# Optimization experiments

Measured on AMD Instinct MI355X. Metric: run time of the kernel, lower is better.

## Reference

```python
import jax, jax.numpy as jnp
import numpy as np

WINDOW_SIZES = (4, 16, 64)
MEMORY_DIM = 256


def setup_inputs() -> dict:
    key = jax.random.key(0)
    ks = jax.random.split(key, 9)
    d_model, mem = 256, MEMORY_DIM
    s_in = 1.0 / np.sqrt(d_model)
    s_mem = 1.0 / np.sqrt(mem)
    return {
        "hidden_states": jax.random.normal(ks[0], (2, 4096, d_model), dtype=jnp.float32),
        # weights stored as (in, out) so projection is x @ W + b
        "Wq": jax.random.normal(ks[1], (d_model, mem), dtype=jnp.float32) * s_in,
        "bq": jax.random.normal(ks[2], (mem,), dtype=jnp.float32) * 0.02,
        "Wk": jax.random.normal(ks[3], (d_model, mem), dtype=jnp.float32) * s_in,
        "bk": jax.random.normal(ks[4], (mem,), dtype=jnp.float32) * 0.02,
        "Wv": jax.random.normal(ks[5], (d_model, mem), dtype=jnp.float32) * s_in,
        "bv": jax.random.normal(ks[6], (mem,), dtype=jnp.float32) * 0.02,
        "Wo": jax.random.normal(ks[7], (mem, d_model), dtype=jnp.float32) * s_mem,
        "bo": jax.random.normal(ks[8], (d_model,), dtype=jnp.float32) * 0.02,
    }


def _gather_patches(h, window):
    # h: (B, L, D). Causal window of `window` positions ending at each l,
    # zero-padded on the left (matches F.pad + unfold in the torch module).
    B, L, D = h.shape
    w = min(window, L)
    padded = jnp.pad(h, ((0, 0), (w - 1, 0), (0, 0)))  # (B, L+w-1, D)
    idx = jnp.arange(L)[:, None] + jnp.arange(w)[None, :]  # (L, w)
    return padded[:, idx]  # (B, L, w, D)


def reference(hidden_states, Wq, bq, Wk, bk, Wv, bv, Wo, bo):
    scale = 1.0 / np.sqrt(MEMORY_DIM)
    q = hidden_states @ Wq + bq  # (B, L, M)
    contexts = []
    for window in WINDOW_SIZES:
        patches = _gather_patches(hidden_states, window)  # (B, L, w, D)
        keys = patches @ Wk + bk      # (B, L, w, M)
        values = patches @ Wv + bv    # (B, L, w, M)
        scores = jnp.einsum('bld,blwd->blw', q, keys) * scale
        attn = jax.nn.softmax(scores, axis=-1)
        contexts.append(jnp.einsum('blw,blwd->bld', attn, values))
    merged = contexts[0]
    for c in contexts[1:]:
        merged = merged + c
    merged = merged / len(contexts)
    return hidden_states + merged @ Wo + bo
```

## Files before the change

### kernel.cpp

```cpp
#include <hip/hip_runtime.h>
#include <hip/hip_bf16.h>

#define D 256
#define NROWS 8192
#define LXK 4160
#define LXV 4176
#define VPAD 64

#define QBLK 16
#define KKEYS 80
#define SSTR 84
#define PSTR 104

typedef unsigned int u32;
typedef unsigned short u16;

typedef short bf16x8 __attribute__((ext_vector_type(8)));
typedef float f32x4 __attribute__((ext_vector_type(4)));

__device__ __forceinline__ u16 f2bf(float f) {
    u32 x = __float_as_uint(f);
    x += 0x7fffu + ((x >> 16) & 1u);
    return (u16)(x >> 16);
}
__device__ __forceinline__ u32 pk2(float a, float b) {
    return (u32)f2bf(a) | ((u32)f2bf(b) << 16);
}

__global__ __launch_bounds__(256) void qkv_mfma(
    const float* __restrict__ H,
    const float* __restrict__ Wq, const float* __restrict__ Wk,
    const float* __restrict__ Wv,
    const float* __restrict__ bq, const float* __restrict__ bkb,
    const float* __restrict__ bvb,
    u16* __restrict__ Qb, u16* __restrict__ Kx, u16* __restrict__ Vt)
{
    __shared__ u16 As[64 * 256];
    __shared__ u16 Bs[2][128 * 68];

    const int tid = threadIdx.x;
    const int bx = blockIdx.x;
    const int by = blockIdx.y;
    const int row0 = by * 64;
    const int mat = bx >> 1;
    const int n0 = (bx & 1) * 128;
    const float* __restrict__ W = (mat == 0) ? Wq : (mat == 1) ? Wk : Wv;

    const int kp = tid >> 3, ng = tid & 7;

    float4 wa[4], wb4[4];
    {
        const float* wr0 = W + (size_t)(kp * 2) * 256 + n0 + ng * 16;
        #pragma unroll
        for (int j = 0; j < 4; ++j) {
            wa[j]  = *(const float4*)(wr0 + j * 4);
            wb4[j] = *(const float4*)(wr0 + 256 + j * 4);
        }
    }
    {
        const int r = tid >> 2, cb = (tid & 3) * 64;
        const float* hp = H + (size_t)(row0 + r) * 256 + cb;
        const int swz = (r & 7) << 3;
        #pragma unroll
        for (int i = 0; i < 16; ++i) {
            float4 h4 = *(const float4*)(hp + i * 4);
            uint2 pv; pv.x = pk2(h4.x, h4.y); pv.y = pk2(h4.z, h4.w);
            *(uint2*)(As + ((r * 256 + cb + i * 4) ^ swz)) = pv;
        }
    }
    {
        u32* bd = (u32*)&Bs[0][0];
        #pragma unroll
        for (int j = 0; j < 4; ++j)
            #pragma unroll
            for (int i = 0; i < 4; ++i)
                bd[(ng * 16 + j * 4 + i) * 34 + kp] = pk2(wa[j][i], wb4[j][i]);
    }
    __syncthreads();

    const int lane = tid & 63, w = tid >> 6;
    const int l15 = lane & 15, lhi = lane >> 4;
    const int rowa = w * 16 + l15;
    const int kb = lhi * 8;
    const int swa = (rowa & 7) << 3;

    bf16x8 af[8];
    #pragma unroll
    for (int ks = 0; ks < 8; ++ks)
        af[ks] = *(const bf16x8*)(As + ((rowa * 256 + ks * 32 + kb) ^ swa));

    f32x4 acc[8];
    #pragma unroll
    for (int i = 0; i < 8; ++i) acc[i] = (f32x4){0.f, 0.f, 0.f, 0.f};

    for (int s = 0; s < 4; ++s) {
        if (s < 3) {
            const float* wr0 = W + (size_t)((s + 1) * 64 + kp * 2) * 256 + n0 + ng * 16;
            #pragma unroll
            for (int j = 0; j < 4; ++j) {
                wa[j]  = *(const float4*)(wr0 + j * 4);
                wb4[j] = *(const float4*)(wr0 + 256 + j * 4);
            }
        }
        #pragma unroll
        for (int ks2 = 0; ks2 < 2; ++ks2) {
            const int ks = s * 2 + ks2;
            #pragma unroll
            for (int i = 0; i < 8; ++i) {
                bf16x8 bf = *(const bf16x8*)&Bs[s & 1][(i * 16 + l15) * 68 + ks2 * 32 + kb];
                acc[i] = __builtin_amdgcn_mfma_f32_16x16x32_bf16(af[ks], bf, acc[i], 0, 0, 0);
            }
        }
        if (s < 3) {
            __syncthreads();
            u32* bd = (u32*)&Bs[(s + 1) & 1][0];
            #pragma unroll
            for (int j = 0; j < 4; ++j)
                #pragma unroll
                for (int i = 0; i < 4; ++i)
                    bd[(ng * 16 + j * 4 + i) * 34 + kp] = pk2(wa[j][i], wb4[j][i]);
            __syncthreads();
        }
    }

    const int batch = row0 >> 12, lr0 = row0 & 4095;

    if (mat == 2) {
        u16* Vtmp = As;
        __syncthreads();
        #pragma unroll
        for (int i = 0; i < 8; ++i) {
            const int dl = i * 16 + l15;
            const float bi = bvb[n0 + dl];
            #pragma unroll
            for (int reg = 0; reg < 4; ++reg) {
                const int key = w * 16 + lhi * 4 + reg;
                Vtmp[dl * 72 + key] = f2bf(acc[i][reg] + bi);
            }
        }
        __syncthreads();
        #pragma unroll
        for (int rep = 0; rep < 2; ++rep) {
            const int dl = rep * 64 + (tid >> 2), q = tid & 3;
            uint4 v0 = *(const uint4*)&Vtmp[dl * 72 + q * 16];
            uint4 v1 = *(const uint4*)&Vtmp[dl * 72 + q * 16 + 8];
            const int gd = n0 + dl;
            u16* dst = Vt + ((size_t)batch * 256 + gd) * LXV + VPAD + lr0 + q * 16;
            *(uint4*)dst = v0;
            *(uint4*)(dst + 8) = v1;
        }
    } else {
        u16* Tq = As;
        const float* bias = (mat == 0) ? bq : bkb;
        __syncthreads();
        #pragma unroll
        for (int i = 0; i < 8; ++i) {
            const int cl = i * 16 + l15;
            const float bi = bias[n0 + cl];
            #pragma unroll
            for (int reg = 0; reg < 4; ++reg)
                Tq[(w * 16 + lhi * 4 + reg) * 136 + cl] = f2bf(acc[i][reg] + bi);
        }
        __syncthreads();
        {
            const int r = tid >> 2, c32 = (tid & 3) * 32;
            uint4 v0 = *(const uint4*)&Tq[r * 136 + c32];
            uint4 v1 = *(const uint4*)&Tq[r * 136 + c32 + 8];
            uint4 v2 = *(const uint4*)&Tq[r * 136 + c32 + 16];
            uint4 v3 = *(const uint4*)&Tq[r * 136 + c32 + 24];
            u16* dst;
            if (mat == 0) dst = Qb + (size_t)(row0 + r) * 256 + n0 + c32;
            else          dst = Kx + ((size_t)batch * LXK + VPAD + lr0 + r) * 256 + n0 + c32;
            *(uint4*)(dst + 0)  = v0;
            *(uint4*)(dst + 8)  = v1;
            *(uint4*)(dst + 16) = v2;
            *(uint4*)(dst + 24) = v3;
        }
    }

    if (bx == 2 && (by & 63) == 0) {
        const int batch2 = by >> 6;
        const int rowp = tid >> 2, c64 = (tid & 3) * 64;
        u16* dst = Kx + ((size_t)batch2 * LXK + rowp) * 256 + c64;
        #pragma unroll
        for (int j = 0; j < 8; ++j) {
            float4 a = *(const float4*)&bkb[c64 + j * 8];
            float4 b = *(const float4*)&bkb[c64 + j * 8 + 4];
            uint4 o;
            o.x = pk2(a.x, a.y); o.y = pk2(a.z, a.w);
            o.z = pk2(b.x, b.y); o.w = pk2(b.z, b.w);
            *(uint4*)(dst + j * 8) = o;
        }
    }
    if (bx == 4 && (by & 63) == 0) {
        const int batch2 = by >> 6;
        const u16 val = f2bf(bvb[tid]);
        const u32 vv = (u32)val | ((u32)val << 16);
        uint4 o; o.x = vv; o.y = vv; o.z = vv; o.w = vv;
        u16* dst = Vt + ((size_t)batch2 * 256 + tid) * LXV;
        #pragma unroll
        for (int j = 0; j < 8; ++j) *(uint4*)(dst + j * 8) = o;
    }
}

__global__ __launch_bounds__(256) void attn_mfma(
    const u16* __restrict__ Qb, const u16* __restrict__ Kx,
    const u16* __restrict__ Vt, u16* __restrict__ Mb)
{
    __shared__ u16 Ks[KKEYS * 256];
    __shared__ float Sb[QBLK * SSTR];
    __shared__ u16 Pb[QBLK * PSTR];

    const int tid = threadIdx.x;
    const int lane = tid & 63, w = tid >> 6;
    const int l15 = lane & 15, lhi = lane >> 4;
    const int r0 = blockIdx.x * QBLK;
    const int batch = r0 >> 12;
    const int lb0 = r0 & 4095;
    const size_t kbase = (size_t)batch * LXK + lb0;

    uint4 kreg[10];
    #pragma unroll
    for (int i = 0; i < 10; ++i) {
        const int u = i * 256 + tid;
        const int row = u >> 5, seg = u & 31;
        kreg[i] = *(const uint4*)&Kx[(kbase + row) * 256 + seg * 8];
    }
    #pragma unroll
    for (int i = 0; i < 10; ++i) {
        const int u = i * 256 + tid;
        const int row = u >> 5, seg = u & 31;
        *(uint4*)&Ks[row * 256 + (seg ^ (row & 7)) * 8] = kreg[i];
    }
    __syncthreads();

    const float scale = 0.0625f;
    const u16* qp = Qb + (size_t)(r0 + l15) * 256;
    bf16x8 qf[8];
    #pragma unroll
    for (int ks = 0; ks < 8; ++ks) qf[ks] = *(const bf16x8*)(qp + ks * 32 + lhi * 8);
    for (int T = w; T < 5; T += 4) {
        const int key = T * 16 + l15;
        f32x4 acc = (f32x4){0.f, 0.f, 0.f, 0.f};
        #pragma unroll
        for (int ks = 0; ks < 8; ++ks) {
            bf16x8 kf = *(const bf16x8*)&Ks[key * 256 + ((ks * 4 + lhi) ^ (key & 7)) * 8];
            acc = __builtin_amdgcn_mfma_f32_16x16x32_bf16(qf[ks], kf, acc, 0, 0, 0);
        }
        #pragma unroll
        for (int reg = 0; reg < 4; ++reg)
            Sb[(lhi * 4 + reg) * SSTR + T * 16 + l15] = acc[reg] * scale;
    }
    __syncthreads();

    {
        const int ri = w * 4 + lhi;
        const int jb = l15;
        float s5[5];
        float m = -1e30f;
        #pragma unroll
        for (int c = 0; c < 5; ++c) {
            const int j = jb + 16 * c;
            const float x = Sb[ri * SSTR + j];
            const bool v = (j >= ri + 1) && (j <= ri + 64);
            s5[c] = v ? x : -1e30f;
            m = fmaxf(m, s5[c]);
        }
        #pragma unroll
        for (int o = 1; o < 16; o <<= 1) m = fmaxf(m, __shfl_xor(m, o));
        float e5[5], z64 = 0.f, z16 = 0.f, z4 = 0.f;
        #pragma unroll
        for (int c = 0; c < 5; ++c) {
            const int j = jb + 16 * c;
            const float e = __expf(s5[c] - m);
            e5[c] = e;
            z64 += e;
            if (j >= ri + 49) z16 += e;
            if (j >= ri + 61) z4 += e;
        }
        #pragma unroll
        for (int o = 1; o < 16; o <<= 1) {
            z64 += __shfl_xor(z64, o);
            z16 += __shfl_xor(z16, o);
            z4  += __shfl_xor(z4, o);
        }
        const float i64 = 1.f / z64, i16 = 1.f / z16, i4 = 1.f / z4;
        #pragma unroll
        for (int c = 0; c < 5; ++c) {
            const int j = jb + 16 * c;
            float wt = e5[c] * (i64 + (j >= ri + 49 ? i16 : 0.f) + (j >= ri + 61 ? i4 : 0.f)) * (1.f / 3.f);
            Pb[ri * PSTR + j] = f2bf(wt);
        }
        Pb[ri * PSTR + 80 + jb] = 0;
    }
    __syncthreads();

    bf16x8 pa[3];
    #pragma unroll
    for (int ks = 0; ks < 3; ++ks)
        pa[ks] = *(const bf16x8*)&Pb[l15 * PSTR + ks * 32 + lhi * 8];
    #pragma unroll
    for (int i = 0; i < 4; ++i) {
        const int dt = w * 4 + i;
        const u16* vrow = Vt + ((size_t)batch * 256 + dt * 16 + l15) * LXV + lb0;
        f32x4 acc = (f32x4){0.f, 0.f, 0.f, 0.f};
        #pragma unroll
        for (int ks = 0; ks < 3; ++ks) {
            bf16x8 vb = *(const bf16x8*)(vrow + ks * 32 + lhi * 8);
            acc = __builtin_amdgcn_mfma_f32_16x16x32_bf16(pa[ks], vb, acc, 0, 0, 0);
        }
        #pragma unroll
        for (int reg = 0; reg < 4; ++reg)
            Mb[(size_t)(r0 + lhi * 4 + reg) * 256 + dt * 16 + l15] = f2bf(acc[reg]);
    }
}

__global__ __launch_bounds__(256) void out_mfma(
    const u16* __restrict__ Mb, const float* __restrict__ Wo,
    const float* __restrict__ bo, const float* __restrict__ H,
    float* __restrict__ out)
{
    __shared__ u16 As[64 * 256];
    __shared__ u16 Bs[2][128 * 68];

    const int tid = threadIdx.x;
    const int bx = blockIdx.x;
    const int by = blockIdx.y;
    const int row0 = by * 64;
    const int n0 = bx * 128;
    const int kp = tid >> 3, ng = tid & 7;

    float4 wa[4], wb4[4];
    {
        const float* wr0 = Wo + (size_t)(kp * 2) * 256 + n0 + ng * 16;
        #pragma unroll
        for (int j = 0; j < 4; ++j) {
            wa[j]  = *(const float4*)(wr0 + j * 4);
            wb4[j] = *(const float4*)(wr0 + 256 + j * 4);
        }
    }
    {
        const int r = tid >> 2, cb = (tid & 3) * 64;
        const u16* mp = Mb + (size_t)(row0 + r) * 256 + cb;
        const int swz = (r & 7) << 3;
        #pragma unroll
        for (int i = 0; i < 8; ++i) {
            uint4 v = *(const uint4*)(mp + i * 8);
            *(uint4*)(As + ((r * 256 + cb + i * 8) ^ swz)) = v;
        }
    }
    {
        u32* bd = (u32*)&Bs[0][0];
        #pragma unroll
        for (int j = 0; j < 4; ++j)
            #pragma unroll
            for (int i = 0; i < 4; ++i)
                bd[(ng * 16 + j * 4 + i) * 34 + kp] = pk2(wa[j][i], wb4[j][i]);
    }
    __syncthreads();

    const int lane = tid & 63, w = tid >> 6;
    const int l15 = lane & 15, lhi = lane >> 4;
    const int rowa = w * 16 + l15;
    const int kb = lhi * 8;
    const int swa = (rowa & 7) << 3;

    bf16x8 af[8];
    #pragma unroll
    for (int ks = 0; ks < 8; ++ks)
        af[ks] = *(const bf16x8*)(As + ((rowa * 256 + ks * 32 + kb) ^ swa));

    f32x4 acc[8];
    #pragma unroll
    for (int i = 0; i < 8; ++i) acc[i] = (f32x4){0.f, 0.f, 0.f, 0.f};

    for (int s = 0; s < 4; ++s) {
        if (s < 3) {
            const float* wr0 = Wo + (size_t)((s + 1) * 64 + kp * 2) * 256 + n0 + ng * 16;
            #pragma unroll
            for (int j = 0; j < 4; ++j) {
                wa[j]  = *(const float4*)(wr0 + j * 4);
                wb4[j] = *(const float4*)(wr0 + 256 + j * 4);
            }
        }
        #pragma unroll
        for (int ks2 = 0; ks2 < 2; ++ks2) {
            const int ks = s * 2 + ks2;
            #pragma unroll
            for (int i = 0; i < 8; ++i) {
                bf16x8 bf = *(const bf16x8*)&Bs[s & 1][(i * 16 + l15) * 68 + ks2 * 32 + kb];
                acc[i] = __builtin_amdgcn_mfma_f32_16x16x32_bf16(af[ks], bf, acc[i], 0, 0, 0);
            }
        }
        if (s < 3) {
            __syncthreads();
            u32* bd = (u32*)&Bs[(s + 1) & 1][0];
            #pragma unroll
            for (int j = 0; j < 4; ++j)
                #pragma unroll
                for (int i = 0; i < 4; ++i)
                    bd[(ng * 16 + j * 4 + i) * 34 + kp] = pk2(wa[j][i], wb4[j][i]);
            __syncthreads();
        }
    }

    #pragma unroll
    for (int i = 0; i < 8; ++i) {
        const int col = n0 + i * 16 + l15;
        const float bi = bo[col];
        #pragma unroll
        for (int reg = 0; reg < 4; ++reg) {
            const int r = row0 + w * 16 + lhi * 4 + reg;
            const size_t off = (size_t)r * 256 + col;
            out[off] = H[off] + acc[i][reg] + bi;
        }
    }
}

extern "C" void kernel_launch(void* const* d_in, const int* in_sizes, int n_in,
                              void* d_out, int out_size, void* d_ws, size_t ws_size,
                              hipStream_t stream) {
    const float* H  = (const float*)d_in[0];
    const float* Wq = (const float*)d_in[1];
    const float* bq = (const float*)d_in[2];
    const float* Wk = (const float*)d_in[3];
    const float* bk = (const float*)d_in[4];
    const float* Wv = (const float*)d_in[5];
    const float* bv = (const float*)d_in[6];
    const float* Wo = (const float*)d_in[7];
    const float* bo = (const float*)d_in[8];
    float* out = (float*)d_out;

    u16* Qb = (u16*)d_ws;
    u16* Kx = Qb + (size_t)NROWS * 256;
    u16* Vt = Kx + (size_t)2 * LXK * 256;
    u16* Mb = Vt + (size_t)2 * 256 * LXV;

    qkv_mfma<<<dim3(6, 128), 256, 0, stream>>>(H, Wq, Wk, Wv, bq, bk, bv, Qb, Kx, Vt);
    attn_mfma<<<512, 256, 0, stream>>>(Qb, Kx, Vt, Mb);
    out_mfma<<<dim3(2, 128), 256, 0, stream>>>(Mb, Wo, bo, H, out);
}
```

Baseline: 51.53 us.

## Fuse output projection into attention kernel, keeping merged context in LDS

Merges the attention kernel and the output-projection GEMM into one kernel. Each 16-row attention block keeps its merged context in shared memory and multiplies it by Wo, which is staged in four 64-row chunks through LDS reused from the key buffer. This removes the Mb round trip through global memory and one kernel launch. In exchange, each of the 512 blocks reloads and converts the whole Wo matrix, which adds global traffic and syncs, and the larger shared-memory footprint may lower occupancy.

```diff
diff --git a/kernel.cpp b/kernel.cpp
--- a/kernel.cpp
+++ b/kernel.cpp
@@ -11,6 +11,7 @@
 #define KKEYS 80
 #define SSTR 84
 #define PSTR 104
+#define MSTR 264
 
 typedef unsigned int u32;
 typedef unsigned short u16;
@@ -203,17 +204,23 @@
     }
 }
 
-__global__ __launch_bounds__(256) void attn_mfma(
+__global__ __launch_bounds__(256) void attn_out(
     const u16* __restrict__ Qb, const u16* __restrict__ Kx,
-    const u16* __restrict__ Vt, u16* __restrict__ Mb)
+    const u16* __restrict__ Vt, const float* __restrict__ Wo,
+    const float* __restrict__ bo, const float* __restrict__ H,
+    float* __restrict__ out)
 {
-    __shared__ u16 Ks[KKEYS * 256];
-    __shared__ float Sb[QBLK * SSTR];
-    __shared__ u16 Pb[QBLK * PSTR];
+    __shared__ __align__(16) char smem[58112];
+    u16*  Ks = (u16*)smem;
+    u16*  Ws = (u16*)smem;
+    float* Sb = (float*)(smem + 40960);
+    u16*  Pb = (u16*)(smem + 46336);
+    u16*  Ml = (u16*)(smem + 49664);
 
     const int tid = threadIdx.x;
     const int lane = tid & 63, w = tid >> 6;
     const int l15 = lane & 15, lhi = lane >> 4;
+    const int kp = tid >> 3, ng = tid & 7;
     const int r0 = blockIdx.x * QBLK;
     const int batch = r0 >> 12;
     const int lb0 = r0 & 4095;
@@ -293,6 +300,19 @@
         }
         Pb[ri * PSTR + 80 + jb] = 0;
     }
+    {
+        const float* wr0 = Wo + (size_t)(kp * 2) * 256 + ng * 32;
+        u32* bd = (u32*)Ws;
+        #pragma unroll
+        for (int j = 0; j < 8; ++j) {
+            float4 a = *(const float4*)(wr0 + j * 4);
+            float4 b = *(const float4*)(wr0 + 256 + j * 4);
+            bd[(ng * 32 + j * 4 + 0) * 34 + kp] = pk2(a.x, b.x);
+            bd[(ng * 32 + j * 4 + 1) * 34 + kp] = pk2(a.y, b.y);
+            bd[(ng * 32 + j * 4 + 2) * 34 + kp] = pk2(a.z, b.z);
+            bd[(ng * 32 + j * 4 + 3) * 34 + kp] = pk2(a.w, b.w);
+        }
+    }
     __syncthreads();
 
     bf16x8 pa[3];
@@ -311,108 +331,54 @@
         }
         #pragma unroll
         for (int reg = 0; reg < 4; ++reg)
-            Mb[(size_t)(r0 + lhi * 4 + reg) * 256 + dt * 16 + l15] = f2bf(acc[reg]);
-    }
-}
-
-__global__ __launch_bounds__(256) void out_mfma(
-    const u16* __restrict__ Mb, const float* __restrict__ Wo,
-    const float* __restrict__ bo, const float* __restrict__ H,
-    float* __restrict__ out)
-{
-    __shared__ u16 As[64 * 256];
-    __shared__ u16 Bs[2][128 * 68];
-
-    const int tid = threadIdx.x;
-    const int bx = blockIdx.x;
-    const int by = blockIdx.y;
-    const int row0 = by * 64;
-    const int n0 = bx * 128;
-    const int kp = tid >> 3, ng = tid & 7;
-
-    float4 wa[4], wb4[4];
-    {
-        const float* wr0 = Wo + (size_t)(kp * 2) * 256 + n0 + ng * 16;
-        #pragma unroll
-        for (int j = 0; j < 4; ++j) {
-            wa[j]  = *(const float4*)(wr0 + j * 4);
-            wb4[j] = *(const float4*)(wr0 + 256 + j * 4);
-        }
-    }
-    {
-        const int r = tid >> 2, cb = (tid & 3) * 64;
-        const u16* mp = Mb + (size_t)(row0 + r) * 256 + cb;
-        const int swz = (r & 7) << 3;
-        #pragma unroll
-        for (int i = 0; i < 8; ++i) {
-            uint4 v = *(const uint4*)(mp + i * 8);
-            *(uint4*)(As + ((r * 256 + cb + i * 8) ^ swz)) = v;
-        }
-    }
-    {
-        u32* bd = (u32*)&Bs[0][0];
-        #pragma unroll
-        for (int j = 0; j < 4; ++j)
-            #pragma unroll
-            for (int i = 0; i < 4; ++i)
-                bd[(ng * 16 + j * 4 + i) * 34 + kp] = pk2(wa[j][i], wb4[j][i]);
+            Ml[(lhi * 4 + reg) * MSTR + dt * 16 + l15] = f2bf(acc[reg]);
     }
     __syncthreads();
 
-    const int lane = tid & 63, w = tid >> 6;
-    const int l15 = lane & 15, lhi = lane >> 4;
-    const int rowa = w * 16 + l15;
-    const int kb = lhi * 8;
-    const int swa = (rowa & 7) << 3;
-
-    bf16x8 af[8];
+    bf16x8 afm[8];
     #pragma unroll
     for (int ks = 0; ks < 8; ++ks)
-        af[ks] = *(const bf16x8*)(As + ((rowa * 256 + ks * 32 + kb) ^ swa));
-
-    f32x4 acc[8];
-    #pragma unroll
-    for (int i = 0; i < 8; ++i) acc[i] = (f32x4){0.f, 0.f, 0.f, 0.f};
+        afm[ks] = *(const bf16x8*)&Ml[l15 * MSTR + ks * 32 + lhi * 8];
+
+    f32x4 oac[4];
+    #pragma unroll
+    for (int t = 0; t < 4; ++t) oac[t] = (f32x4){0.f, 0.f, 0.f, 0.f};
 
     for (int s = 0; s < 4; ++s) {
-        if (s < 3) {
-            const float* wr0 = Wo + (size_t)((s + 1) * 64 + kp * 2) * 256 + n0 + ng * 16;
-            #pragma unroll
-            for (int j = 0; j < 4; ++j) {
-                wa[j]  = *(const float4*)(wr0 + j * 4);
-                wb4[j] = *(const float4*)(wr0 + 256 + j * 4);
+        if (s > 0) {
+            __syncthreads();
+            const float* wr0 = Wo + (size_t)(s * 64 + kp * 2) * 256 + ng * 32;
+            u32* bd = (u32*)Ws;
+            #pragma unroll
+            for (int j = 0; j < 8; ++j) {
+                float4 a = *(const float4*)(wr0 + j * 4);
+                float4 b = *(const float4*)(wr0 + 256 + j * 4);
+                bd[(ng * 32 + j * 4 + 0) * 34 + kp] = pk2(a.x, b.x);
+                bd[(ng * 32 + j * 4 + 1) * 34 + kp] = pk2(a.y, b.y);
+                bd[(ng * 32 + j * 4 + 2) * 34 + kp] = pk2(a.z, b.z);
+                bd[(ng * 32 + j * 4 + 3) * 34 + kp] = pk2(a.w, b.w);
             }
+            __syncthreads();
         }
         #pragma unroll
         for (int ks2 = 0; ks2 < 2; ++ks2) {
-            const int ks = s * 2 + ks2;
-            #pragma unroll
-            for (int i = 0; i < 8; ++i) {
-                bf16x8 bf = *(const bf16x8*)&Bs[s & 1][(i * 16 + l15) * 68 + ks2 * 32 + kb];
-                acc[i] = __builtin_amdgcn_mfma_f32_16x16x32_bf16(af[ks], bf, acc[i], 0, 0, 0);
+            #pragma unroll
+            for (int t = 0; t < 4; ++t) {
+                bf16x8 bf = *(const bf16x8*)&Ws[((w * 4 + t) * 16 + l15) * 68 + ks2 * 32 + lhi * 8];
+                oac[t] = __builtin_amdgcn_mfma_f32_16x16x32_bf16(afm[s * 2 + ks2], bf, oac[t], 0, 0, 0);
             }
         }
-        if (s < 3) {
-            __syncthreads();
-            u32* bd = (u32*)&Bs[(s + 1) & 1][0];
-            #pragma unroll
-            for (int j = 0; j < 4; ++j)
-                #pragma unroll
-                for (int i = 0; i < 4; ++i)
-                    bd[(ng * 16 + j * 4 + i) * 34 + kp] = pk2(wa[j][i], wb4[j][i]);
-            __syncthreads();
-        }
-    }
-
-    #pragma unroll
-    for (int i = 0; i < 8; ++i) {
-        const int col = n0 + i * 16 + l15;
+    }
+
+    #pragma unroll
+    for (int t = 0; t < 4; ++t) {
+        const int col = w * 64 + t * 16 + l15;
         const float bi = bo[col];
         #pragma unroll
         for (int reg = 0; reg < 4; ++reg) {
-            const int r = row0 + w * 16 + lhi * 4 + reg;
+            const int r = r0 + lhi * 4 + reg;
             const size_t off = (size_t)r * 256 + col;
-            out[off] = H[off] + acc[i][reg] + bi;
+            out[off] = H[off] + oac[t][reg] + bi;
         }
     }
 }
@@ -434,9 +400,7 @@
     u16* Qb = (u16*)d_ws;
     u16* Kx = Qb + (size_t)NROWS * 256;
     u16* Vt = Kx + (size_t)2 * LXK * 256;
-    u16* Mb = Vt + (size_t)2 * 256 * LXV;
 
     qkv_mfma<<<dim3(6, 128), 256, 0, stream>>>(H, Wq, Wk, Wv, bq, bk, bv, Qb, Kx, Vt);
-    attn_mfma<<<512, 256, 0, stream>>>(Qb, Kx, Vt, Mb);
-    out_mfma<<<dim3(2, 128), 256, 0, stream>>>(Mb, Wo, bo, H, out);
+    attn_out<<<512, 256, 0, stream>>>(Qb, Kx, Vt, Wo, bo, H, out);
 }
```

Result: slower. 111.5 us (+116.4%).
